# Performance work log

Hardware: AMD Instinct MI355X
Metric: run time of the kernel (lower is better)

The kernel has to match this reference:

```python
import jax, jax.numpy as jnp
import numpy as np

D_MODEL = 1024
N_HEADS = 16
D_FF = 4096
EPS = 1e-5


def setup_inputs() -> dict:
    key = jax.random.key(0)
    ks = jax.random.split(key, 13)
    d, f = D_MODEL, D_FF
    s = 1.0 / np.sqrt(d)
    sf = 1.0 / np.sqrt(f)
    return {
        "x": jax.random.normal(ks[0], (2, 2048, d), dtype=jnp.float32),
        "Wq": jax.random.normal(ks[1], (d, d), dtype=jnp.float32) * s,
        "bq": jnp.zeros((d,), jnp.float32),
        "Wk": jax.random.normal(ks[2], (d, d), dtype=jnp.float32) * s,
        "bk": jnp.zeros((d,), jnp.float32),
        "Wv": jax.random.normal(ks[3], (d, d), dtype=jnp.float32) * s,
        "bv": jnp.zeros((d,), jnp.float32),
        "Wo": jax.random.normal(ks[4], (d, d), dtype=jnp.float32) * s,
        "bo": jnp.zeros((d,), jnp.float32),
        "W1": jax.random.normal(ks[5], (f, d), dtype=jnp.float32) * s,
        "b1": jnp.zeros((f,), jnp.float32),
        "W2": jax.random.normal(ks[6], (d, f), dtype=jnp.float32) * sf,
        "b2": jnp.zeros((d,), jnp.float32),
        "g1": jnp.ones((d,), jnp.float32),
        "be1": jnp.zeros((d,), jnp.float32),
        "g2": jnp.ones((d,), jnp.float32),
        "be2": jnp.zeros((d,), jnp.float32),
    }


def _layernorm(x, g, b):
    mu = jnp.mean(x, axis=-1, keepdims=True)
    var = jnp.mean(jnp.square(x - mu), axis=-1, keepdims=True)
    return (x - mu) * jax.lax.rsqrt(var + EPS) * g + b


def reference(x, Wq, bq, Wk, bk, Wv, bv, Wo, bo, W1, b1, W2, b2, g1, be1, g2, be2):
    B, S, D = x.shape
    H = N_HEADS
    dk = D // H
    # QKV projections (torch Linear: x @ W.T + b), reshape to [B,H,S,dk]
    def proj(W, b):
        return (x @ W.T + b).reshape(B, S, H, dk).transpose(0, 2, 1, 3)
    Q, K, V = proj(Wq, bq), proj(Wk, bk), proj(Wv, bv)
    scores = jnp.einsum("bhsd,bhtd->bhst", Q, K) / jnp.sqrt(jnp.float32(dk))
    attn = jax.nn.softmax(scores, axis=-1)
    ctx = jnp.einsum("bhst,bhtd->bhsd", attn, V)
    ctx = ctx.transpose(0, 2, 1, 3).reshape(B, S, D)
    attn_out = ctx @ Wo.T + bo
    x1 = _layernorm(x + attn_out, g1, be1)
    ff = jax.nn.relu(x1 @ W1.T + b1) @ W2.T + b2
    return _layernorm(x1 + ff, g2, be2)
```

## Files before the change

### kernel.cpp

```cpp
#include <hip/hip_runtime.h>

typedef unsigned short u16;
typedef unsigned int u32;
typedef unsigned long long u64;
typedef __attribute__((ext_vector_type(8))) short short8;
typedef __attribute__((ext_vector_type(4))) float f32x4;

#define D_MODEL 1024
#define SEQ 2048
#define NH 16
#define DK 64
#define DFF 4096
#define NTOK 4096
#define LOG2E 1.44269504f

__device__ __forceinline__ u16 f2bf(float f) {
    unsigned x = __builtin_bit_cast(unsigned, f);
    x = x + 0x7fffu + ((x >> 16) & 1u);
    return (u16)(x >> 16);
}

__device__ __forceinline__ float bf2f(u16 v) {
    return __builtin_bit_cast(float, (u32)v << 16);
}

__device__ __forceinline__ float fexp2(float x) {
    float r;
    asm("v_exp_f32 %0, %1" : "=v"(r) : "v"(x));
    return r;
}

__device__ __forceinline__ void gload_lds16(const void* g, void* l) {
    __builtin_amdgcn_global_load_lds(
        (__attribute__((address_space(1))) void*)g,
        (__attribute__((address_space(3))) void*)l, 16, 0, 0);
}

__device__ __forceinline__ void cvt_body(const float* __restrict__ in,
                                         u16* __restrict__ out, int blk) {
    size_t i = ((size_t)blk * 256 + threadIdx.x) * 4;
    float4 v = *(const float4*)(in + i);
    out[i + 0] = f2bf(v.x);
    out[i + 1] = f2bf(v.y);
    out[i + 2] = f2bf(v.z);
    out[i + 3] = f2bf(v.w);
}

__global__ __launch_bounds__(256) void cvt_all(
    const float* __restrict__ sx, const float* __restrict__ s0,
    const float* __restrict__ s1, const float* __restrict__ s2,
    const float* __restrict__ s3, const float* __restrict__ s4,
    const float* __restrict__ s5, u16* __restrict__ dx, u16* __restrict__ d0,
    u16* __restrict__ d1, u16* __restrict__ d2, u16* __restrict__ d3,
    u16* __restrict__ d4, u16* __restrict__ d5) {
    int f = blockIdx.x;
    if (f < 4096) {
        cvt_body(sx, dx, f);
    } else if (f < 8192) {
        int which = (f - 4096) >> 10, blk = (f - 4096) & 1023;
        const float* s = which == 0 ? s0 : which == 1 ? s1 : which == 2 ? s2 : s3;
        u16* d = which == 0 ? d0 : which == 1 ? d1 : which == 2 ? d2 : d3;
        cvt_body(s, d, blk);
    } else if (f < 12288) {
        cvt_body(s4, d4, f - 8192);
    } else {
        cvt_body(s5, d5, f - 12288);
    }
}

__device__ __forceinline__ void gemm_core64(const u16* __restrict__ A,
                                            const u16* __restrict__ W, int K,
                                            int m0, int n0, int kbase, int kl,
                                            f32x4 (&acc)[2][4]) {
    __shared__ short8 As[64][8];
    __shared__ short8 Bs[128][8];
    const int tid = threadIdx.x;
    const int lane = tid & 63, w = tid >> 6;
    const int l15 = lane & 15, lg = lane >> 4;
    const int wr = (w >> 1) * 32, wc = (w & 1) * 64;
    const int psw = l15 & 7;

#pragma unroll
    for (int i = 0; i < 2; ++i)
#pragma unroll
        for (int jj = 0; jj < 4; ++jj) acc[i][jj] = (f32x4){0.f, 0.f, 0.f, 0.f};

    for (int k0 = kbase; k0 < kbase + kl; k0 += 64) {
        __syncthreads();
#pragma unroll
        for (int jj = 0; jj < 2; ++jj) {
            int idx = jj * 256 + tid;
            int r = idx >> 3, ck = idx & 7;
            gload_lds16(A + (size_t)(m0 + r) * K + k0 + ((ck ^ (r & 7)) * 8),
                        (char*)As + (jj * 256 + w * 64) * 16);
        }
#pragma unroll
        for (int jj = 0; jj < 4; ++jj) {
            int idx = jj * 256 + tid;
            int r = idx >> 3, ck = idx & 7;
            gload_lds16(W + (size_t)(n0 + r) * K + k0 + ((ck ^ (r & 7)) * 8),
                        (char*)Bs + (jj * 256 + w * 64) * 16);
        }
        __syncthreads();

#pragma unroll
        for (int kk = 0; kk < 2; ++kk) {
            short8 af[2], bf[4];
#pragma unroll
            for (int m = 0; m < 2; ++m)
                af[m] = As[wr + m * 16 + l15][(kk * 4 + lg) ^ psw];
#pragma unroll
            for (int nn = 0; nn < 4; ++nn)
                bf[nn] = Bs[wc + nn * 16 + l15][(kk * 4 + lg) ^ psw];
#pragma unroll
            for (int m = 0; m < 2; ++m)
#pragma unroll
                for (int nn = 0; nn < 4; ++nn)
                    acc[m][nn] = __builtin_amdgcn_mfma_f32_16x16x32_bf16(
                        af[m], bf[nn], acc[m][nn], 0, 0, 0);
        }
    }
}

__global__ __launch_bounds__(256) void gemm_k64(
    const u16* __restrict__ A, const u16* __restrict__ W,
    const float* __restrict__ bias, u16* __restrict__ outb,
    u16* __restrict__ outb2, int M, int N, int K, int KZ) {
    const int f = blockIdx.x;
    const int xcd = f & 7, j = f >> 3;
    const int mi = j & 7, n = (j >> 3) & 7, kz = j >> 6;
    const int m0 = (xcd * 8 + mi) * 64, n0 = n * 128;
    const int kl = K / KZ, kbase = kz * kl;
    u16* out = kz ? outb2 : outb;

    f32x4 acc[2][4];
    gemm_core64(A, W, K, m0, n0, kbase, kl, acc);

    const int lane = threadIdx.x & 63, w = threadIdx.x >> 6;
    const int l15 = lane & 15, lg = lane >> 4;
    const int wr = (w >> 1) * 32, wc = (w & 1) * 64;
#pragma unroll
    for (int m = 0; m < 2; ++m)
#pragma unroll
        for (int nn = 0; nn < 4; ++nn) {
            int gn = n0 + wc + nn * 16 + l15;
            float bv = (kz == 0) ? bias[gn] : 0.f;
#pragma unroll
            for (int r = 0; r < 4; ++r) {
                int gm = m0 + wr + m * 16 + lg * 4 + r;
                out[(size_t)gm * N + gn] = f2bf(acc[m][nn][r] + bv);
            }
        }
}

__global__ __launch_bounds__(256) void gemm_k64_relu(
    const u16* __restrict__ A, const u16* __restrict__ W,
    const float* __restrict__ bias, u16* __restrict__ outb, int M, int N,
    int K) {
    const int f = blockIdx.x;
    const int xcd = f & 7, j = f >> 3;
    const int mi = j & 7, n = j >> 3;
    const int m0 = (xcd * 8 + mi) * 64, n0 = n * 128;

    f32x4 acc[2][4];
    gemm_core64(A, W, K, m0, n0, 0, K, acc);

    const int lane = threadIdx.x & 63, w = threadIdx.x >> 6;
    const int l15 = lane & 15, lg = lane >> 4;
    const int wr = (w >> 1) * 32, wc = (w & 1) * 64;
#pragma unroll
    for (int m = 0; m < 2; ++m)
#pragma unroll
        for (int nn = 0; nn < 4; ++nn) {
            int gn = n0 + wc + nn * 16 + l15;
            float bv = bias[gn];
#pragma unroll
            for (int r = 0; r < 4; ++r) {
                int gm = m0 + wr + m * 16 + lg * 4 + r;
                outb[(size_t)gm * N + gn] = f2bf(fmaxf(acc[m][nn][r] + bv, 0.f));
            }
        }
}

__global__ __launch_bounds__(256) void gemm_qkv(
    const u16* __restrict__ A, const u16* __restrict__ Wq,
    const u16* __restrict__ Wk, const u16* __restrict__ Wv,
    const float* __restrict__ bq, const float* __restrict__ bk,
    const float* __restrict__ bv, u16* __restrict__ Qo, u16* __restrict__ Ko,
    u16* __restrict__ Vo) {
    const int f = blockIdx.x;
    const int xcd = f & 7, j = f >> 3;
    const int mi = j & 7, q = j >> 3;
    const int mat = q >> 3;
    const int m0 = (xcd * 8 + mi) * 64, n0 = (q & 7) * 128;
    const u16* W = mat == 0 ? Wq : (mat == 1 ? Wk : Wv);
    const float* bias = mat == 0 ? bq : (mat == 1 ? bk : bv);
    const float scale = (mat == 0) ? 0.125f * LOG2E : 1.0f;

    f32x4 acc[2][4];
    gemm_core64(A, W, D_MODEL, m0, n0, 0, D_MODEL, acc);

    const int lane = threadIdx.x & 63, w = threadIdx.x >> 6;
    const int l15 = lane & 15, lg = lane >> 4;
    const int wr = (w >> 1) * 32, wc = (w & 1) * 64;

    if (mat == 2) {
#pragma unroll
        for (int m = 0; m < 2; ++m)
#pragma unroll
            for (int nn = 0; nn < 4; ++nn) {
                int gn = n0 + wc + nn * 16 + l15;
                float bv2 = bias[gn];
                int h = gn >> 6, d = gn & 63;
                int gm0 = m0 + wr + m * 16 + lg * 4;
                int b = gm0 >> 11, s = gm0 & 2047;
                u64 pk = (u64)f2bf(acc[m][nn][0] + bv2) |
                         ((u64)f2bf(acc[m][nn][1] + bv2) << 16) |
                         ((u64)f2bf(acc[m][nn][2] + bv2) << 32) |
                         ((u64)f2bf(acc[m][nn][3] + bv2) << 48);
                size_t obase = (size_t)(b * NH + h) * DK * SEQ;
                int soff = (s & ~63) + ((((s >> 3) & 7) ^ (d & 7)) << 3) + (s & 7);
                *(u64*)(Vo + obase + (size_t)d * SEQ + soff) = pk;
            }
    } else {
        u16* out = mat == 0 ? Qo : Ko;
#pragma unroll
        for (int m = 0; m < 2; ++m)
#pragma unroll
            for (int nn = 0; nn < 4; ++nn) {
                int gn = n0 + wc + nn * 16 + l15;
                float bv2 = bias[gn];
                int h = gn >> 6, d = gn & 63;
#pragma unroll
                for (int r = 0; r < 4; ++r) {
                    int gm = m0 + wr + m * 16 + lg * 4 + r;
                    int b = gm >> 11, s = gm & 2047;
                    float v = (acc[m][nn][r] + bv2) * scale;
                    out[(((size_t)(b * NH + h)) * SEQ + s) * DK + d] = f2bf(v);
                }
            }
    }
}

#define KVB 64
__global__ __launch_bounds__(512) void attn_fwd(const u16* __restrict__ Q,
                                                const u16* __restrict__ Kp,
                                                const u16* __restrict__ Vg_,
                                                u16* __restrict__ ctx) {
    __shared__ __align__(16) u16 Kt[2][64 * 64];
    __shared__ __align__(16) u16 Vt[2][64 * 64];
    __shared__ __align__(16) u16 Ps[8][16 * 64];

    const int tid = threadIdx.x;
    const int lane = tid & 63;
    const int w = tid >> 6;
    const int l15 = lane & 15;
    const int lg = lane >> 4;
    const int f = blockIdx.x + 16 * blockIdx.y;
    const int bh = f & 31;
    const int qblk = f >> 5;
    const int qbase = qblk * 128 + w * 16;
    const u16* Qb = Q + (size_t)bh * SEQ * DK;
    const u16* Kb = Kp + (size_t)bh * SEQ * DK;
    const u16* Vg = Vg_ + (size_t)bh * DK * SEQ;

    short8 qf[2];
#pragma unroll
    for (int hf = 0; hf < 2; ++hf)
        qf[hf] = *(const short8*)(Qb + (size_t)(qbase + l15) * DK + hf * 32 + lg * 8);

    short8 onesf;
#pragma unroll
    for (int e = 0; e < 8; ++e) onesf[e] = (short)0x3F80;

    f32x4 zero = {0.f, 0.f, 0.f, 0.f};
    f32x4 o[4], o1 = zero;
#pragma unroll
    for (int db = 0; db < 4; ++db) o[db] = zero;
    float m_own = 0.f;

    u16* Pu = Ps[w];
    const int psw = l15 & 7;

#define STAGE_V(T0, BUF)                                                       \
    {                                                                          \
        gload_lds16(Vg + (size_t)(tid >> 3) * SEQ + (T0) + (tid & 7) * 8,      \
                    (char*)Vt[BUF] + (w * 64) * 16);                           \
    }
#define STAGE_K(T0, BUF)                                                       \
    {                                                                          \
        int kv = tid >> 3, ck = tid & 7;                                       \
        gload_lds16(Kb + (size_t)((T0) + kv) * DK + ((ck ^ (kv & 7)) * 8),     \
                    (char*)Kt[BUF] + (w * 64) * 16);                           \
    }
#define KF(BUF, NB, HALF)                                                      \
    (*(const short8*)((const char*)Kt[BUF] + ((NB)*16 + l15) * 128 +           \
                      (((((HALF)*4 + lg)) ^ psw) << 4)))

#define ATTN_TILE(BUF)                                                         \
    {                                                                          \
        f32x4 seed = {-m_own, -m_own, -m_own, -m_own};                         \
        f32x4 sc[4];                                                           \
        __builtin_amdgcn_s_setprio(1);                                         \
        _Pragma("unroll") for (int nb = 0; nb < 4; ++nb) {                     \
            sc[nb] = __builtin_amdgcn_mfma_f32_16x16x32_bf16(                  \
                KF(BUF, nb, 0), qf[0], seed, 0, 0, 0);                         \
            sc[nb] = __builtin_amdgcn_mfma_f32_16x16x32_bf16(                  \
                KF(BUF, nb, 1), qf[1], sc[nb], 0, 0, 0);                       \
        }                                                                      \
        __builtin_amdgcn_s_setprio(0);                                         \
        float a0 = fmaxf(fmaxf(sc[0][0], sc[0][1]), sc[0][2]);                 \
        float a1 = fmaxf(fmaxf(sc[0][3], sc[1][0]), sc[1][1]);                 \
        float a2 = fmaxf(fmaxf(sc[1][2], sc[1][3]), sc[2][0]);                 \
        float a3 = fmaxf(fmaxf(sc[2][1], sc[2][2]), sc[2][3]);                 \
        float a4 = fmaxf(fmaxf(sc[3][0], sc[3][1]), sc[3][2]);                 \
        float lm = fmaxf(fmaxf(fmaxf(a0, a1), a2),                             \
                         fmaxf(fmaxf(a3, a4), sc[3][3]));                      \
        if (__any(lm > 8.f)) {                                                 \
            float rv = fmaxf(lm, __shfl_xor(lm, 16));                          \
            rv = fmaxf(rv, __shfl_xor(rv, 32));                                \
            float rvp = fmaxf(rv, 0.f);                                        \
            float fac = fexp2(-rvp);                                           \
            m_own += rvp;                                                      \
            _Pragma("unroll") for (int nb = 0; nb < 4; ++nb)                   \
                _Pragma("unroll") for (int r = 0; r < 4; ++r)                  \
                    sc[nb][r] -= rvp;                                          \
            _Pragma("unroll") for (int r = 0; r < 4; ++r) {                    \
                float fr = __shfl(fac, lg * 4 + r);                            \
                o1[r] *= fr;                                                   \
                _Pragma("unroll") for (int db = 0; db < 4; ++db)               \
                    o[db][r] *= fr;                                            \
            }                                                                  \
        }                                                                      \
        _Pragma("unroll") for (int nb = 0; nb < 4; ++nb) {                     \
            float p0 = fexp2(sc[nb][0]);                                       \
            float p1 = fexp2(sc[nb][1]);                                       \
            float p2 = fexp2(sc[nb][2]);                                       \
            float p3 = fexp2(sc[nb][3]);                                       \
            u32 pk01 = __builtin_amdgcn_perm(__builtin_bit_cast(u32, p1),      \
                                             __builtin_bit_cast(u32, p0),      \
                                             0x07060302u);                     \
            u32 pk23 = __builtin_amdgcn_perm(__builtin_bit_cast(u32, p3),      \
                                             __builtin_bit_cast(u32, p2),      \
                                             0x07060302u);                     \
            int ck = (nb * 2 + (lg >> 1)) ^ psw;                               \
            u64* dst = (u64*)(Pu + l15 * 64 + ck * 8 + (lg & 1) * 4);          \
            *dst = (u64)pk01 | ((u64)pk23 << 32);                              \
        }                                                                      \
        short8 pa[2];                                                          \
        _Pragma("unroll") for (int ts = 0; ts < 2; ++ts)                       \
            pa[ts] = *(const short8*)(Pu + l15 * 64 + (((ts * 4 + lg) ^ psw) * 8)); \
        __builtin_amdgcn_s_setprio(1);                                         \
        _Pragma("unroll") for (int db = 0; db < 4; ++db) {                     \
            const int d = db * 16 + l15;                                       \
            _Pragma("unroll") for (int ts = 0; ts < 2; ++ts) {                 \
                short8 vb = *(const short8*)((const char*)Vt[BUF] + d * 128 +  \
                                             (((ts * 4 + lg) ^ psw) << 4));    \
                o[db] = __builtin_amdgcn_mfma_f32_16x16x32_bf16(               \
                    pa[ts], vb, o[db], 0, 0, 0);                               \
            }                                                                  \
        }                                                                      \
        o1 = __builtin_amdgcn_mfma_f32_16x16x32_bf16(pa[0], onesf, o1, 0, 0, 0); \
        o1 = __builtin_amdgcn_mfma_f32_16x16x32_bf16(pa[1], onesf, o1, 0, 0, 0); \
        __builtin_amdgcn_s_setprio(0);                                         \
    }

    STAGE_K(0, 0);
    STAGE_V(0, 0);

    for (int t0 = 0; t0 < SEQ; t0 += 2 * KVB) {
        __syncthreads();
        STAGE_K(t0 + KVB, 1);
        STAGE_V(t0 + KVB, 1);
        ATTN_TILE(0);
        __syncthreads();
        if (t0 + 2 * KVB < SEQ) {
            STAGE_K(t0 + 2 * KVB, 0);
            STAGE_V(t0 + 2 * KVB, 0);
        }
        ATTN_TILE(1);
    }

    const int b = bh >> 4, h = bh & 15;
#pragma unroll
    for (int r = 0; r < 4; ++r) {
        float inv = 1.0f / o1[r];
        int srow = qbase + lg * 4 + r;
        size_t rowoff = ((size_t)(b * SEQ + srow)) * D_MODEL + h * DK;
#pragma unroll
        for (int db = 0; db < 4; ++db)
            ctx[rowoff + db * 16 + l15] = f2bf(o[db][r] * inv);
    }
#undef STAGE_V
#undef STAGE_K
#undef KF
#undef ATTN_TILE
}

template <bool XBF>
__global__ __launch_bounds__(256) void ln_res(const void* __restrict__ Xv,
                                              const u16* __restrict__ Y,
                                              const u16* __restrict__ Y2,
                                              const float* __restrict__ gamma,
                                              const float* __restrict__ beta,
                                              float* __restrict__ outf,
                                              u16* __restrict__ outb) {
    __shared__ float red[8];
    const int row = blockIdx.x, t = threadIdx.x;
    const size_t off = (size_t)row * D_MODEL + t * 4;
    float x0, x1_, x2, x3;
    if (XBF) {
        ushort4 xv = *(const ushort4*)((const u16*)Xv + off);
        x0 = bf2f(xv.x); x1_ = bf2f(xv.y); x2 = bf2f(xv.z); x3 = bf2f(xv.w);
    } else {
        float4 xv = *(const float4*)((const float*)Xv + off);
        x0 = xv.x; x1_ = xv.y; x2 = xv.z; x3 = xv.w;
    }
    ushort4 yv = *(const ushort4*)(Y + off);
    float sx = x0 + bf2f(yv.x), sy = x1_ + bf2f(yv.y);
    float sz = x2 + bf2f(yv.z), sw = x3 + bf2f(yv.w);
    if (Y2) {
        ushort4 y2 = *(const ushort4*)(Y2 + off);
        sx += bf2f(y2.x); sy += bf2f(y2.y); sz += bf2f(y2.z); sw += bf2f(y2.w);
    }
    float ps = sx + sy + sz + sw;
#pragma unroll
    for (int o2 = 32; o2; o2 >>= 1) ps += __shfl_xor(ps, o2);
    if ((t & 63) == 0) red[t >> 6] = ps;
    __syncthreads();
    float mu = (red[0] + red[1] + red[2] + red[3]) * (1.0f / D_MODEL);
    float d0 = sx - mu, d1 = sy - mu, d2 = sz - mu, d3 = sw - mu;
    float p2 = d0 * d0 + d1 * d1 + d2 * d2 + d3 * d3;
#pragma unroll
    for (int o2 = 32; o2; o2 >>= 1) p2 += __shfl_xor(p2, o2);
    if ((t & 63) == 0) red[4 + (t >> 6)] = p2;
    __syncthreads();
    float var = (red[4] + red[5] + red[6] + red[7]) * (1.0f / D_MODEL);
    float rstd = rsqrtf(var + 1e-5f);
    float4 gv = *(const float4*)(gamma + t * 4);
    float4 bv = *(const float4*)(beta + t * 4);
    float r0 = d0 * rstd * gv.x + bv.x;
    float r1 = d1 * rstd * gv.y + bv.y;
    float r2 = d2 * rstd * gv.z + bv.z;
    float r3 = d3 * rstd * gv.w + bv.w;
    if (outf) {
        float4 res; res.x = r0; res.y = r1; res.z = r2; res.w = r3;
        *(float4*)(outf + off) = res;
    }
    if (outb) {
        outb[off + 0] = f2bf(r0);
        outb[off + 1] = f2bf(r1);
        outb[off + 2] = f2bf(r2);
        outb[off + 3] = f2bf(r3);
    }
}

extern "C" void kernel_launch(void* const* d_in, const int* in_sizes, int n_in,
                              void* d_out, int out_size, void* d_ws, size_t ws_size,
                              hipStream_t stream) {
    (void)in_sizes; (void)n_in; (void)out_size; (void)ws_size;
    const float* x  = (const float*)d_in[0];
    const float* Wq = (const float*)d_in[1];
    const float* bq = (const float*)d_in[2];
    const float* Wk = (const float*)d_in[3];
    const float* bk = (const float*)d_in[4];
    const float* Wv = (const float*)d_in[5];
    const float* bv = (const float*)d_in[6];
    const float* Wo = (const float*)d_in[7];
    const float* bo = (const float*)d_in[8];
    const float* W1 = (const float*)d_in[9];
    const float* b1 = (const float*)d_in[10];
    const float* W2 = (const float*)d_in[11];
    const float* b2 = (const float*)d_in[12];
    const float* g1 = (const float*)d_in[13];
    const float* be1 = (const float*)d_in[14];
    const float* g2 = (const float*)d_in[15];
    const float* be2 = (const float*)d_in[16];

    char* ws = (char*)d_ws;
    u16* xb   = (u16*)(ws);
    u16* Qb   = (u16*)(ws + ((size_t)8 << 20));
    u16* Kb   = (u16*)(ws + ((size_t)16 << 20));
    u16* x1b  = (u16*)(ws + ((size_t)24 << 20));
    u16* W1b  = (u16*)(ws + ((size_t)32 << 20));
    u16* W2b  = (u16*)(ws + ((size_t)40 << 20));
    u16* Fs   = (u16*)(ws + ((size_t)48 << 20));
    u16* Fs2  = (u16*)(ws + ((size_t)56 << 20));
    u16* hb   = (u16*)(ws + ((size_t)64 << 20));
    u16* Wqb = hb;
    u16* Wkb = hb + (1u << 20);
    u16* Wvb = hb + (2u << 20);
    u16* Wob = hb + (3u << 20);
    u16* Vtg = Fs;
    u16* ctxb = xb;

    cvt_all<<<dim3(16384), 256, 0, stream>>>(x, Wq, Wk, Wv, Wo, W1, W2,
                                             xb, Wqb, Wkb, Wvb, Wob, W1b, W2b);

    gemm_qkv<<<dim3(1536), 256, 0, stream>>>(xb, Wqb, Wkb, Wvb, bq, bk, bv,
                                             Qb, Kb, Vtg);

    attn_fwd<<<dim3(SEQ / 128, 32), 512, 0, stream>>>(Qb, Kb, Vtg, ctxb);

    gemm_k64<<<dim3(1024), 256, 0, stream>>>(ctxb, Wob, bo, Fs, Fs2,
                                             NTOK, D_MODEL, D_MODEL, 2);

    ln_res<false><<<dim3(NTOK), 256, 0, stream>>>(x, Fs, Fs2, g1, be1,
                                                  nullptr, x1b);

    gemm_k64_relu<<<dim3(2048), 256, 0, stream>>>(x1b, W1b, b1, hb,
                                                  NTOK, DFF, D_MODEL);

    gemm_k64<<<dim3(1024), 256, 0, stream>>>(hb, W2b, b2, Fs, Fs2,
                                             NTOK, D_MODEL, DFF, 2);

    ln_res<true><<<dim3(NTOK), 256, 0, stream>>>(x1b, Fs, Fs2, g2, be2,
                                                 (float*)d_out, nullptr);
}
```

Before: 221.2 us.

## Double-buffer LDS tiles in gemm_core64 to overlap global loads with MFMA

Splits the shared A/B tiles into two buffers and restructures the K loop to process 128 elements per iteration. The next 64-wide slice is staged into the idle buffer while the MFMAs consume the current one, so global-to-LDS traffic overlaps with compute instead of being serialized by barriers. The cost is twice the LDS per block and a loop that assumes the per-split K length is a multiple of 128.

```diff
diff --git a/kernel.cpp b/kernel.cpp
--- a/kernel.cpp
+++ b/kernel.cpp
@@ -72,8 +72,8 @@
                                             const u16* __restrict__ W, int K,
                                             int m0, int n0, int kbase, int kl,
                                             f32x4 (&acc)[2][4]) {
-    __shared__ short8 As[64][8];
-    __shared__ short8 Bs[128][8];
+    __shared__ short8 As[2][64][8];
+    __shared__ short8 Bs[2][128][8];
     const int tid = threadIdx.x;
     const int lane = tid & 63, w = tid >> 6;
     const int l15 = lane & 15, lg = lane >> 4;
@@ -85,41 +85,47 @@
 #pragma unroll
         for (int jj = 0; jj < 4; ++jj) acc[i][jj] = (f32x4){0.f, 0.f, 0.f, 0.f};
 
-    for (int k0 = kbase; k0 < kbase + kl; k0 += 64) {
+#define STAGE64(B_, K0)                                                        \
+    {                                                                          \
+        _Pragma("unroll") for (int jj = 0; jj < 2; ++jj) {                     \
+            int idx = jj * 256 + tid;                                          \
+            int r = idx >> 3, ck = idx & 7;                                    \
+            gload_lds16(A + (size_t)(m0 + r) * K + (K0) + ((ck ^ (r & 7)) * 8),\
+                        (char*)As[B_] + (jj * 256 + w * 64) * 16);             \
+        }                                                                      \
+        _Pragma("unroll") for (int jj = 0; jj < 4; ++jj) {                     \
+            int idx = jj * 256 + tid;                                          \
+            int r = idx >> 3, ck = idx & 7;                                    \
+            gload_lds16(W + (size_t)(n0 + r) * K + (K0) + ((ck ^ (r & 7)) * 8),\
+                        (char*)Bs[B_] + (jj * 256 + w * 64) * 16);             \
+        }                                                                      \
+    }
+#define COMP64(B_)                                                             \
+    {                                                                          \
+        _Pragma("unroll") for (int kk = 0; kk < 2; ++kk) {                     \
+            short8 af[2], bf[4];                                               \
+            _Pragma("unroll") for (int m = 0; m < 2; ++m)                      \
+                af[m] = As[B_][wr + m * 16 + l15][(kk * 4 + lg) ^ psw];        \
+            _Pragma("unroll") for (int nn = 0; nn < 4; ++nn)                   \
+                bf[nn] = Bs[B_][wc + nn * 16 + l15][(kk * 4 + lg) ^ psw];      \
+            _Pragma("unroll") for (int m = 0; m < 2; ++m)                      \
+                _Pragma("unroll") for (int nn = 0; nn < 4; ++nn)               \
+                    acc[m][nn] = __builtin_amdgcn_mfma_f32_16x16x32_bf16(      \
+                        af[m], bf[nn], acc[m][nn], 0, 0, 0);                   \
+        }                                                                      \
+    }
+
+    STAGE64(0, kbase);
+    for (int k0 = kbase; k0 < kbase + kl; k0 += 128) {
         __syncthreads();
-#pragma unroll
-        for (int jj = 0; jj < 2; ++jj) {
-            int idx = jj * 256 + tid;
-            int r = idx >> 3, ck = idx & 7;
-            gload_lds16(A + (size_t)(m0 + r) * K + k0 + ((ck ^ (r & 7)) * 8),
-                        (char*)As + (jj * 256 + w * 64) * 16);
-        }
-#pragma unroll
-        for (int jj = 0; jj < 4; ++jj) {
-            int idx = jj * 256 + tid;
-            int r = idx >> 3, ck = idx & 7;
-            gload_lds16(W + (size_t)(n0 + r) * K + k0 + ((ck ^ (r & 7)) * 8),
-                        (char*)Bs + (jj * 256 + w * 64) * 16);
-        }
+        STAGE64(1, k0 + 64);
+        COMP64(0);
         __syncthreads();
-
-#pragma unroll
-        for (int kk = 0; kk < 2; ++kk) {
-            short8 af[2], bf[4];
-#pragma unroll
-            for (int m = 0; m < 2; ++m)
-                af[m] = As[wr + m * 16 + l15][(kk * 4 + lg) ^ psw];
-#pragma unroll
-            for (int nn = 0; nn < 4; ++nn)
-                bf[nn] = Bs[wc + nn * 16 + l15][(kk * 4 + lg) ^ psw];
-#pragma unroll
-            for (int m = 0; m < 2; ++m)
-#pragma unroll
-                for (int nn = 0; nn < 4; ++nn)
-                    acc[m][nn] = __builtin_amdgcn_mfma_f32_16x16x32_bf16(
-                        af[m], bf[nn], acc[m][nn], 0, 0, 0);
-        }
-    }
+        if (k0 + 128 < kbase + kl) STAGE64(0, k0 + 128);
+        COMP64(1);
+    }
+#undef STAGE64
+#undef COMP64
 }
 
 __global__ __launch_bounds__(256) void gemm_k64(
```

Result: slower. 247.0 us (+11.6%).

## Process two query sub-tiles per wave in attention to reuse K/V fragments

Applied to the files above, without the earlier changes.

Halves the attention block to 4 waves, with each wave handling 32 query rows as two 16-row sub-tiles that share the K and V fragments loaded from LDS. Each thread now stages two 16-byte chunks of K and V per tile. The aim is to cut LDS reads per MFMA and give each wave more independent MFMA work to interleave. In exchange it roughly doubles accumulator and score registers per wave and reduces waves per block, which may lower occupancy and latency hiding.

```diff
diff --git a/kernel.cpp b/kernel.cpp
--- a/kernel.cpp
+++ b/kernel.cpp
@@ -243,13 +243,13 @@
 }
 
 #define KVB 64
-__global__ __launch_bounds__(512) void attn_fwd(const u16* __restrict__ Q,
-                                                const u16* __restrict__ Kp,
-                                                const u16* __restrict__ Vg_,
-                                                u16* __restrict__ ctx) {
+__global__ __launch_bounds__(256, 3) void attn_fwd(const u16* __restrict__ Q,
+                                                   const u16* __restrict__ Kp,
+                                                   const u16* __restrict__ Vg_,
+                                                   u16* __restrict__ ctx) {
     __shared__ __align__(16) u16 Kt[2][64 * 64];
     __shared__ __align__(16) u16 Vt[2][64 * 64];
-    __shared__ __align__(16) u16 Ps[8][16 * 64];
+    __shared__ __align__(16) u16 Ps[4][2][16 * 64];
 
     const int tid = threadIdx.x;
     const int lane = tid & 63;
@@ -259,84 +259,83 @@
     const int f = blockIdx.x + 16 * blockIdx.y;
     const int bh = f & 31;
     const int qblk = f >> 5;
-    const int qbase = qblk * 128 + w * 16;
+    const int qbase = qblk * 128 + w * 32;
     const u16* Qb = Q + (size_t)bh * SEQ * DK;
     const u16* Kb = Kp + (size_t)bh * SEQ * DK;
     const u16* Vg = Vg_ + (size_t)bh * DK * SEQ;
 
-    short8 qf[2];
-#pragma unroll
-    for (int hf = 0; hf < 2; ++hf)
-        qf[hf] = *(const short8*)(Qb + (size_t)(qbase + l15) * DK + hf * 32 + lg * 8);
+    short8 qfA[2], qfB[2];
+#pragma unroll
+    for (int hf = 0; hf < 2; ++hf) {
+        qfA[hf] = *(const short8*)(Qb + (size_t)(qbase + l15) * DK + hf * 32 + lg * 8);
+        qfB[hf] = *(const short8*)(Qb + (size_t)(qbase + 16 + l15) * DK + hf * 32 + lg * 8);
+    }
 
     short8 onesf;
 #pragma unroll
     for (int e = 0; e < 8; ++e) onesf[e] = (short)0x3F80;
 
     f32x4 zero = {0.f, 0.f, 0.f, 0.f};
-    f32x4 o[4], o1 = zero;
-#pragma unroll
-    for (int db = 0; db < 4; ++db) o[db] = zero;
-    float m_own = 0.f;
-
-    u16* Pu = Ps[w];
+    f32x4 oA[4], oB[4], s1A = zero, s1B = zero;
+#pragma unroll
+    for (int db = 0; db < 4; ++db) { oA[db] = zero; oB[db] = zero; }
+    float mA = 0.f, mB = 0.f;
+
+    u16* PuA = Ps[w][0];
+    u16* PuB = Ps[w][1];
     const int psw = l15 & 7;
 
 #define STAGE_V(T0, BUF)                                                       \
     {                                                                          \
-        gload_lds16(Vg + (size_t)(tid >> 3) * SEQ + (T0) + (tid & 7) * 8,      \
-                    (char*)Vt[BUF] + (w * 64) * 16);                           \
+        _Pragma("unroll") for (int j = 0; j < 2; ++j) {                        \
+            int idx = j * 256 + tid;                                           \
+            gload_lds16(Vg + (size_t)(idx >> 3) * SEQ + (T0) + (idx & 7) * 8,  \
+                        (char*)Vt[BUF] + (j * 256 + w * 64) * 16);             \
+        }                                                                      \
     }
 #define STAGE_K(T0, BUF)                                                       \
     {                                                                          \
-        int kv = tid >> 3, ck = tid & 7;                                       \
-        gload_lds16(Kb + (size_t)((T0) + kv) * DK + ((ck ^ (kv & 7)) * 8),     \
-                    (char*)Kt[BUF] + (w * 64) * 16);                           \
+        _Pragma("unroll") for (int j = 0; j < 2; ++j) {                        \
+            int idx = j * 256 + tid;                                           \
+            int kv = idx >> 3, ck = idx & 7;                                   \
+            gload_lds16(Kb + (size_t)((T0) + kv) * DK + ((ck ^ (kv & 7)) * 8), \
+                        (char*)Kt[BUF] + (j * 256 + w * 64) * 16);             \
+        }                                                                      \
     }
 #define KF(BUF, NB, HALF)                                                      \
     (*(const short8*)((const char*)Kt[BUF] + ((NB)*16 + l15) * 128 +           \
                       (((((HALF)*4 + lg)) ^ psw) << 4)))
 
-#define ATTN_TILE(BUF)                                                         \
+#define SOFTMAX(SC, MOWN, OO, SS, PU)                                          \
     {                                                                          \
-        f32x4 seed = {-m_own, -m_own, -m_own, -m_own};                         \
-        f32x4 sc[4];                                                           \
-        __builtin_amdgcn_s_setprio(1);                                         \
-        _Pragma("unroll") for (int nb = 0; nb < 4; ++nb) {                     \
-            sc[nb] = __builtin_amdgcn_mfma_f32_16x16x32_bf16(                  \
-                KF(BUF, nb, 0), qf[0], seed, 0, 0, 0);                         \
-            sc[nb] = __builtin_amdgcn_mfma_f32_16x16x32_bf16(                  \
-                KF(BUF, nb, 1), qf[1], sc[nb], 0, 0, 0);                       \
-        }                                                                      \
-        __builtin_amdgcn_s_setprio(0);                                         \
-        float a0 = fmaxf(fmaxf(sc[0][0], sc[0][1]), sc[0][2]);                 \
-        float a1 = fmaxf(fmaxf(sc[0][3], sc[1][0]), sc[1][1]);                 \
-        float a2 = fmaxf(fmaxf(sc[1][2], sc[1][3]), sc[2][0]);                 \
-        float a3 = fmaxf(fmaxf(sc[2][1], sc[2][2]), sc[2][3]);                 \
-        float a4 = fmaxf(fmaxf(sc[3][0], sc[3][1]), sc[3][2]);                 \
+        float a0 = fmaxf(fmaxf(SC[0][0], SC[0][1]), SC[0][2]);                 \
+        float a1 = fmaxf(fmaxf(SC[0][3], SC[1][0]), SC[1][1]);                 \
+        float a2 = fmaxf(fmaxf(SC[1][2], SC[1][3]), SC[2][0]);                 \
+        float a3 = fmaxf(fmaxf(SC[2][1], SC[2][2]), SC[2][3]);                 \
+        float a4 = fmaxf(fmaxf(SC[3][0], SC[3][1]), SC[3][2]);                 \
         float lm = fmaxf(fmaxf(fmaxf(a0, a1), a2),                             \
-                         fmaxf(fmaxf(a3, a4), sc[3][3]));                      \
+                         fmaxf(fmaxf(a3, a4), SC[3][3]));                      \
         if (__any(lm > 8.f)) {                                                 \
             float rv = fmaxf(lm, __shfl_xor(lm, 16));                          \
             rv = fmaxf(rv, __shfl_xor(rv, 32));                                \
             float rvp = fmaxf(rv, 0.f);                                        \
             float fac = fexp2(-rvp);                                           \
-            m_own += rvp;                                                      \
+            MOWN += rvp;                                                       \
             _Pragma("unroll") for (int nb = 0; nb < 4; ++nb)                   \
                 _Pragma("unroll") for (int r = 0; r < 4; ++r)                  \
-                    sc[nb][r] -= rvp;                                          \
+                    SC[nb][r] -= rvp;                                          \
             _Pragma("unroll") for (int r = 0; r < 4; ++r) {                    \
                 float fr = __shfl(fac, lg * 4 + r);                            \
-                o1[r] *= fr;                                                   \
+                SS[r] *= fr;                                                   \
                 _Pragma("unroll") for (int db = 0; db < 4; ++db)               \
-                    o[db][r] *= fr;                                            \
+                    OO[db][r] *= fr;                                           \
             }                                                                  \
         }                                                                      \
         _Pragma("unroll") for (int nb = 0; nb < 4; ++nb) {                     \
-            float p0 = fexp2(sc[nb][0]);                                       \
-            float p1 = fexp2(sc[nb][1]);                                       \
-            float p2 = fexp2(sc[nb][2]);                                       \
-            float p3 = fexp2(sc[nb][3]);                                       \
+            float p0 = fexp2(SC[nb][0]);                                       \
+            float p1 = fexp2(SC[nb][1]);                                       \
+            float p2 = fexp2(SC[nb][2]);                                       \
+            float p3 = fexp2(SC[nb][3]);                                       \
             u32 pk01 = __builtin_amdgcn_perm(__builtin_bit_cast(u32, p1),      \
                                              __builtin_bit_cast(u32, p0),      \
                                              0x07060302u);                     \
@@ -344,24 +343,55 @@
                                              __builtin_bit_cast(u32, p2),      \
                                              0x07060302u);                     \
             int ck = (nb * 2 + (lg >> 1)) ^ psw;                               \
-            u64* dst = (u64*)(Pu + l15 * 64 + ck * 8 + (lg & 1) * 4);          \
+            u64* dst = (u64*)(PU + l15 * 64 + ck * 8 + (lg & 1) * 4);          \
             *dst = (u64)pk01 | ((u64)pk23 << 32);                              \
         }                                                                      \
-        short8 pa[2];                                                          \
-        _Pragma("unroll") for (int ts = 0; ts < 2; ++ts)                       \
-            pa[ts] = *(const short8*)(Pu + l15 * 64 + (((ts * 4 + lg) ^ psw) * 8)); \
+    }
+
+#define ATTN_TILE(BUF)                                                         \
+    {                                                                          \
+        f32x4 seedA = {-mA, -mA, -mA, -mA};                                    \
+        f32x4 seedB = {-mB, -mB, -mB, -mB};                                    \
+        f32x4 scA[4], scB[4];                                                  \
+        __builtin_amdgcn_s_setprio(1);                                         \
+        _Pragma("unroll") for (int nb = 0; nb < 4; ++nb) {                     \
+            short8 k0 = KF(BUF, nb, 0);                                        \
+            short8 k1 = KF(BUF, nb, 1);                                        \
+            scA[nb] = __builtin_amdgcn_mfma_f32_16x16x32_bf16(                 \
+                k0, qfA[0], seedA, 0, 0, 0);                                   \
+            scA[nb] = __builtin_amdgcn_mfma_f32_16x16x32_bf16(                 \
+                k1, qfA[1], scA[nb], 0, 0, 0);                                 \
+            scB[nb] = __builtin_amdgcn_mfma_f32_16x16x32_bf16(                 \
+                k0, qfB[0], seedB, 0, 0, 0);                                   \
+            scB[nb] = __builtin_amdgcn_mfma_f32_16x16x32_bf16(                 \
+                k1, qfB[1], scB[nb], 0, 0, 0);                                 \
+        }                                                                      \
+        __builtin_amdgcn_s_setprio(0);                                         \
+        SOFTMAX(scA, mA, oA, s1A, PuA)                                         \
+        SOFTMAX(scB, mB, oB, s1B, PuB)                                         \
+        short8 paA[2], paB[2];                                                 \
+        _Pragma("unroll") for (int ts = 0; ts < 2; ++ts) {                     \
+            paA[ts] = *(const short8*)(PuA + l15 * 64 +                        \
+                                       (((ts * 4 + lg) ^ psw) * 8));           \
+            paB[ts] = *(const short8*)(PuB + l15 * 64 +                        \
+                                       (((ts * 4 + lg) ^ psw) * 8));           \
+        }                                                                      \
         __builtin_amdgcn_s_setprio(1);                                         \
         _Pragma("unroll") for (int db = 0; db < 4; ++db) {                     \
             const int d = db * 16 + l15;                                       \
             _Pragma("unroll") for (int ts = 0; ts < 2; ++ts) {                 \
                 short8 vb = *(const short8*)((const char*)Vt[BUF] + d * 128 +  \
                                              (((ts * 4 + lg) ^ psw) << 4));    \
-                o[db] = __builtin_amdgcn_mfma_f32_16x16x32_bf16(               \
-                    pa[ts], vb, o[db], 0, 0, 0);                               \
+                oA[db] = __builtin_amdgcn_mfma_f32_16x16x32_bf16(              \
+                    paA[ts], vb, oA[db], 0, 0, 0);                             \
+                oB[db] = __builtin_amdgcn_mfma_f32_16x16x32_bf16(              \
+                    paB[ts], vb, oB[db], 0, 0, 0);                             \
             }                                                                  \
         }                                                                      \
-        o1 = __builtin_amdgcn_mfma_f32_16x16x32_bf16(pa[0], onesf, o1, 0, 0, 0); \
-        o1 = __builtin_amdgcn_mfma_f32_16x16x32_bf16(pa[1], onesf, o1, 0, 0, 0); \
+        s1A = __builtin_amdgcn_mfma_f32_16x16x32_bf16(paA[0], onesf, s1A, 0, 0, 0); \
+        s1A = __builtin_amdgcn_mfma_f32_16x16x32_bf16(paA[1], onesf, s1A, 0, 0, 0); \
+        s1B = __builtin_amdgcn_mfma_f32_16x16x32_bf16(paB[0], onesf, s1B, 0, 0, 0); \
+        s1B = __builtin_amdgcn_mfma_f32_16x16x32_bf16(paB[1], onesf, s1B, 0, 0, 0); \
         __builtin_amdgcn_s_setprio(0);                                         \
     }
 
@@ -384,16 +414,22 @@
     const int b = bh >> 4, h = bh & 15;
 #pragma unroll
     for (int r = 0; r < 4; ++r) {
-        float inv = 1.0f / o1[r];
-        int srow = qbase + lg * 4 + r;
-        size_t rowoff = ((size_t)(b * SEQ + srow)) * D_MODEL + h * DK;
-#pragma unroll
-        for (int db = 0; db < 4; ++db)
-            ctx[rowoff + db * 16 + l15] = f2bf(o[db][r] * inv);
+        float invA = 1.0f / s1A[r];
+        float invB = 1.0f / s1B[r];
+        int srowA = qbase + lg * 4 + r;
+        int srowB = qbase + 16 + lg * 4 + r;
+        size_t rowA = ((size_t)(b * SEQ + srowA)) * D_MODEL + h * DK;
+        size_t rowB = ((size_t)(b * SEQ + srowB)) * D_MODEL + h * DK;
+#pragma unroll
+        for (int db = 0; db < 4; ++db) {
+            ctx[rowA + db * 16 + l15] = f2bf(oA[db][r] * invA);
+            ctx[rowB + db * 16 + l15] = f2bf(oB[db][r] * invB);
+        }
     }
 #undef STAGE_V
 #undef STAGE_K
 #undef KF
+#undef SOFTMAX
 #undef ATTN_TILE
 }
 
@@ -500,7 +536,7 @@
     gemm_qkv<<<dim3(1536), 256, 0, stream>>>(xb, Wqb, Wkb, Wvb, bq, bk, bv,
                                              Qb, Kb, Vtg);
 
-    attn_fwd<<<dim3(SEQ / 128, 32), 512, 0, stream>>>(Qb, Kb, Vtg, ctxb);
+    attn_fwd<<<dim3(SEQ / 128, 32), 256, 0, stream>>>(Qb, Kb, Vtg, ctxb);
 
     gemm_k64<<<dim3(1024), 256, 0, stream>>>(ctxb, Wob, bo, Fs, Fs2,
                                              NTOK, D_MODEL, D_MODEL, 2);
```

Measured after the change: 225.2 us. Within noise of the previous version (+1.8%).
